# Performance work log

Hardware: AMD Instinct MI355X
Metric: run time of the kernel (lower is better)

Reference implementation:

```python
import jax, jax.numpy as jnp
import numpy as np
import math

EMBED_DIM = 1024
NUM_HEADS = 16
HEAD_DIM = EMBED_DIM // NUM_HEADS
B, S = 2, 2048


def setup_inputs() -> dict:
    key = jax.random.key(0)
    ks = jax.random.split(key, 5)
    scale = 1.0 / math.sqrt(EMBED_DIM)
    x = jax.random.normal(ks[0], (B, S, EMBED_DIM), dtype=jnp.float32)
    W_q = jax.random.normal(ks[1], (EMBED_DIM, EMBED_DIM), dtype=jnp.float32) * scale
    W_k = jax.random.normal(ks[2], (EMBED_DIM, EMBED_DIM), dtype=jnp.float32) * scale
    W_v = jax.random.normal(ks[3], (EMBED_DIM, EMBED_DIM), dtype=jnp.float32) * scale
    W_o = jax.random.normal(ks[4], (EMBED_DIM, EMBED_DIM), dtype=jnp.float32) * scale
    # causal mask: True = masked out (matches torch masked_fill semantics)
    mask = jnp.triu(jnp.ones((S, S), dtype=bool), k=1)
    return {"x": x, "mask": mask, "W_q": W_q, "W_k": W_k, "W_v": W_v, "W_o": W_o}


def _split_heads(x):
    b, s, _ = x.shape
    return x.reshape(b, s, NUM_HEADS, HEAD_DIM).transpose(0, 2, 1, 3)  # [b,h,s,hd]


def reference(x, mask, W_q, W_k, W_v, W_o):
    # torch nn.Linear(bias=False): y = x @ W.T
    Q = _split_heads(x @ W_q.T)
    K = _split_heads(x @ W_k.T)
    V = _split_heads(x @ W_v.T)
    scale = 1.0 / math.sqrt(HEAD_DIM)
    scores = jnp.einsum("bhqd,bhkd->bhqk", Q, K) * scale  # [b,h,s,s]
    scores = jnp.where(mask[None, None, :, :], -jnp.inf, scores)
    weights = jax.nn.softmax(scores, axis=-1)
    out = jnp.einsum("bhqk,bhkd->bhqd", weights, V)
    out = out.transpose(0, 2, 1, 3).reshape(x.shape[0], x.shape[1], EMBED_DIM)
    return out @ W_o.T
```

## Files before the change

### kernel.cpp

```cpp
#include <hip/hip_runtime.h>
#include <hip/hip_bf16.h>

typedef short bf16x8 __attribute__((ext_vector_type(8)));
typedef unsigned short u16x8 __attribute__((ext_vector_type(8)));
typedef float f32x4 __attribute__((ext_vector_type(4)));

typedef unsigned int __attribute__((address_space(1))) gu32;
typedef unsigned int __attribute__((address_space(3))) lu32;

#define MFMA16(a, b, c) __builtin_amdgcn_mfma_f32_16x16x32_bf16((a), (b), (c), 0, 0, 0)

constexpr int SEQ = 2048;
constexpr int NH = 16;
constexpr int NTOK = 2 * SEQ;

__device__ __forceinline__ float bf2f(unsigned short u) {
  union { unsigned int i; float f; } v; v.i = ((unsigned int)u) << 16; return v.f;
}
__device__ __forceinline__ unsigned short f2bf(float f) {
  __hip_bfloat16 h = __float2bfloat16(f);
  return __builtin_bit_cast(unsigned short, h);
}
__device__ __forceinline__ u16x8 cvt8(const float* __restrict__ p) {
  f32x4 a = *(const f32x4*)p;
  f32x4 b = *(const f32x4*)(p + 4);
  u16x8 r;
#pragma unroll
  for (int j = 0; j < 4; j++) { r[j] = f2bf(a[j]); r[4 + j] = f2bf(b[j]); }
  return r;
}

__global__ __launch_bounds__(256) void cvt_all(
    const float* __restrict__ x, const float* __restrict__ wq, const float* __restrict__ wk,
    const float* __restrict__ wv, const float* __restrict__ wo,
    unsigned short* __restrict__ Xb, unsigned short* __restrict__ Wb) {
  const int z = blockIdx.y;
  const float* src = (z == 0) ? x : (z == 1) ? wq : (z == 2) ? wk : (z == 3) ? wv : wo;
  unsigned short* dst = (z == 0) ? Xb : Wb + (size_t)(z - 1) * 1024 * 1024;
  const int n = (z == 0) ? NTOK * 1024 : 1024 * 1024;
  for (int i = (blockIdx.x * 256 + threadIdx.x) * 8; i < n; i += gridDim.x * 256 * 8)
    *(u16x8*)(dst + i) = cvt8(src + i);
}

template <int ROWS, int NWAVE>
__device__ __forceinline__ void stage_glds(const unsigned short* __restrict__ gbase,
                                           int rstride,
                                           unsigned short* __restrict__ lds,
                                           int wid, int lane) {
  constexpr int ISS = ROWS * 8 / (NWAVE * 64);
#pragma unroll
  for (int t = 0; t < ISS; ++t) {
    const int slot = (wid * ISS + t) * 64 + lane;
    const int row = slot >> 3;
    const int c8 = (slot & 7) ^ (row & 7);
    const unsigned short* gp = gbase + (size_t)row * rstride + c8 * 8;
    unsigned short* lp = lds + (size_t)(wid * ISS + t) * 512;
    __builtin_amdgcn_global_load_lds((const gu32*)gp, (lu32*)lp, 16, 0, 0);
  }
}

__device__ __forceinline__ bf16x8 frag_ld(const unsigned short* __restrict__ lds, int row, int c8) {
  const int slot = row * 8 + (c8 ^ (row & 7));
  return *(const bf16x8*)(lds + slot * 8);
}

template <int BM, int BN, int LDC, bool CF32>
__global__ __launch_bounds__(256) void gemm_lds(
    const unsigned short* __restrict__ A,
    const unsigned short* __restrict__ B,
    void* __restrict__ Cv) {
  constexpr int K = 1024;
  constexpr int MI = BM / 32, NI = BN / 32;

  __shared__ __align__(16) unsigned short As[BM * 64];
  __shared__ __align__(16) unsigned short Bs[BN * 64];

  const int tid = threadIdx.x;
  const int wid = tid >> 6;
  const int lane = tid & 63;
  const int quad = lane >> 4;
  const int c16 = lane & 15;
  const int wrow = wid >> 1, wcol = wid & 1;

  const int m0 = blockIdx.y * BM;
  const int n0 = blockIdx.x * BN;
  const unsigned short* Bz = B + (size_t)blockIdx.z * 1024 * 1024;
  const int cofs = blockIdx.z * 1024;

  f32x4 acc[MI][NI];
#pragma unroll
  for (int i = 0; i < MI; i++)
#pragma unroll
    for (int j = 0; j < NI; j++) acc[i][j] = f32x4{0.f, 0.f, 0.f, 0.f};

  for (int kb = 0; kb < K; kb += 64) {
    __syncthreads();
    stage_glds<BM, 4>(A + (size_t)m0 * K + kb, K, As, wid, lane);
    stage_glds<BN, 4>(Bz + (size_t)n0 * K + kb, K, Bs, wid, lane);
    __syncthreads();
#pragma unroll
    for (int ks = 0; ks < 2; ++ks) {
      bf16x8 af[MI], bfr[NI];
#pragma unroll
      for (int i = 0; i < MI; i++)
        af[i] = frag_ld(As, wrow * (BM / 2) + i * 16 + c16, ks * 4 + quad);
#pragma unroll
      for (int j = 0; j < NI; j++)
        bfr[j] = frag_ld(Bs, wcol * (BN / 2) + j * 16 + c16, ks * 4 + quad);
#pragma unroll
      for (int i = 0; i < MI; i++)
#pragma unroll
        for (int j = 0; j < NI; j++) acc[i][j] = MFMA16(af[i], bfr[j], acc[i][j]);
    }
  }

#pragma unroll
  for (int i = 0; i < MI; i++) {
#pragma unroll
    for (int j = 0; j < NI; j++) {
      int row = m0 + wrow * (BM / 2) + i * 16 + quad * 4;
      int col = n0 + wcol * (BN / 2) + j * 16 + c16 + cofs;
#pragma unroll
      for (int r = 0; r < 4; r++) {
        if constexpr (CF32) ((float*)Cv)[(size_t)(row + r) * LDC + col] = acc[i][j][r];
        else ((unsigned short*)Cv)[(size_t)(row + r) * LDC + col] = f2bf(acc[i][j][r]);
      }
    }
  }
}

__device__ __forceinline__ int vt_idx(int d, int kv) {
  int ck = kv >> 3;
  int s = ((d >> 3) ^ d) & 7;
  return d * 64 + ((ck ^ s) << 3) + (kv & 7);
}

struct AttnShared {
  unsigned short Kt[2][64 * 64];
  unsigned short Vt[2][64 * 64];
  unsigned short Pt[64][72];
};

__device__ __forceinline__ void attn_phase(
    AttnShared& sh, const unsigned short* __restrict__ QKV,
    unsigned short* __restrict__ Oa, size_t tokbase, int h, int q0, int nkv,
    int tid, int wid, int lane, int quad, int c16) {
  __syncthreads();

  const unsigned short* qp = QKV + (tokbase + q0 + wid * 16 + c16) * 3072 + h * 64;
  bf16x8 qf[2];
#pragma unroll
  for (int ks = 0; ks < 2; ++ks) {
    u16x8 u = *(const u16x8*)(qp + ks * 32 + quad * 8);
    bf16x8 t;
#pragma unroll
    for (int j = 0; j < 8; j++) t[j] = (short)f2bf(0.1803368801f * bf2f(u[j]));
    qf[ks] = t;
  }

  const unsigned short* kbase = QKV + tokbase * 3072 + 1024 + h * 64;
  const unsigned short* vbase = QKV + tokbase * 3072 + 2048 + h * 64;
  const int vrp = tid >> 3, vc8 = tid & 7;

  f32x4 o[4];
  float lacc[4];
#pragma unroll
  for (int nt = 0; nt < 4; nt++) o[nt] = f32x4{0.f, 0.f, 0.f, 0.f};
#pragma unroll
  for (int r = 0; r < 4; r++) lacc[r] = 0.f;

  stage_glds<64, 4>(kbase, 3072, sh.Kt[0], wid, lane);
  u16x8 vr0 = *(const u16x8*)(vbase + (size_t)(vrp * 2) * 3072 + vc8 * 8);
  u16x8 vr1 = *(const u16x8*)(vbase + (size_t)(vrp * 2 + 1) * 3072 + vc8 * 8);

  for (int kt = 0; kt < nkv; ++kt) {
    const int buf = kt & 1;
#pragma unroll
    for (int j = 0; j < 8; j++) {
      unsigned int w = (unsigned int)vr0[j] | ((unsigned int)vr1[j] << 16);
      *(unsigned int*)&sh.Vt[buf][vt_idx(vc8 * 8 + j, vrp * 2)] = w;
    }
    __syncthreads();

    if (kt + 1 < nkv) {
      const size_t nofs = (size_t)(kt + 1) * 64;
      stage_glds<64, 4>(kbase + nofs * 3072, 3072, sh.Kt[buf ^ 1], wid, lane);
      vr0 = *(const u16x8*)(vbase + (nofs + vrp * 2) * 3072 + vc8 * 8);
      vr1 = *(const u16x8*)(vbase + (nofs + vrp * 2 + 1) * 3072 + vc8 * 8);
    }

    const unsigned short* KtB = sh.Kt[buf];
    const unsigned short* VtB = sh.Vt[buf];
    f32x4 s[4];
#pragma unroll
    for (int nt = 0; nt < 4; ++nt) {
      f32x4 a = f32x4{-16.f, -16.f, -16.f, -16.f};
      a = MFMA16(qf[0], frag_ld(KtB, nt * 16 + c16, quad), a);
      a = MFMA16(qf[1], frag_ld(KtB, nt * 16 + c16, 4 + quad), a);
      s[nt] = a;
    }
    if (kt == nkv - 1) {
#pragma unroll
      for (int nt = 0; nt < 4; nt++)
#pragma unroll
        for (int r = 0; r < 4; r++) {
          int qg = wid * 16 + quad * 4 + r;
          int kg = nt * 16 + c16;
          if (kg > qg) s[nt][r] = -1e30f;
        }
    }

#pragma unroll
    for (int nt = 0; nt < 4; nt++) {
#pragma unroll
      for (int r = 0; r < 4; r++) {
        float p = exp2f(s[nt][r]);
        lacc[r] += p;
        sh.Pt[wid * 16 + quad * 4 + r][nt * 16 + c16] = f2bf(p);
      }
    }

#pragma unroll
    for (int ks = 0; ks < 2; ++ks) {
      bf16x8 pf = *(const bf16x8*)&sh.Pt[wid * 16 + c16][ks * 32 + quad * 8];
#pragma unroll
      for (int nt = 0; nt < 4; ++nt) {
        bf16x8 vf = *(const bf16x8*)&VtB[vt_idx(nt * 16 + c16, ks * 32 + quad * 8)];
        o[nt] = MFMA16(pf, vf, o[nt]);
      }
    }
  }

#pragma unroll
  for (int r = 0; r < 4; r++) {
#pragma unroll
    for (int off = 1; off < 16; off <<= 1) lacc[r] += __shfl_xor(lacc[r], off);
    lacc[r] = 1.f / lacc[r];
  }
#pragma unroll
  for (int nt = 0; nt < 4; nt++) {
#pragma unroll
    for (int r = 0; r < 4; r++) {
      int row = q0 + wid * 16 + quad * 4 + r;
      int col = h * 64 + nt * 16 + c16;
      Oa[(tokbase + row) * 1024 + col] = f2bf(o[nt][r] * lacc[r]);
    }
  }
}

__global__ __launch_bounds__(256) void attn_kernel(
    const unsigned short* __restrict__ QKV,
    unsigned short* __restrict__ Oa) {
  __shared__ AttnShared sh;
  const int pr = blockIdx.x;
  const int h = blockIdx.y;
  const int b = blockIdx.z;
  const int tid = threadIdx.x;
  const int wid = tid >> 6, lane = tid & 63;
  const int quad = lane >> 4, c16 = lane & 15;
  const size_t tokbase = (size_t)b * SEQ;

  attn_phase(sh, QKV, Oa, tokbase, h, (31 - pr) * 64, 32 - pr, tid, wid, lane, quad, c16);
  attn_phase(sh, QKV, Oa, tokbase, h, pr * 64, pr + 1, tid, wid, lane, quad, c16);
}

template <int BM, int BN, int LDC, bool AF32, bool CF32>
__global__ __launch_bounds__(256) void gemm_bt(
    const void* __restrict__ Av, const float* __restrict__ W0, const float* __restrict__ W1,
    const float* __restrict__ W2, void* __restrict__ Cv) {
  constexpr int K = 1024;
  constexpr int LDS_LD = 72;
  constexpr int MI = BM / 32, NI = BN / 32;
  __shared__ __align__(16) unsigned short As[BM][LDS_LD];
  __shared__ __align__(16) unsigned short Bs[BN][LDS_LD];
  const int tid = threadIdx.x, wid = tid >> 6, lane = tid & 63;
  const int quad = lane >> 4, c16 = lane & 15;
  const int wrow = wid >> 1, wcol = wid & 1;
  const float* W = (blockIdx.z == 0) ? W0 : (blockIdx.z == 1 ? W1 : W2);
  const int m0 = blockIdx.y * BM, n0 = blockIdx.x * BN, cofs = blockIdx.z * 1024;
  f32x4 acc[MI][NI];
#pragma unroll
  for (int i = 0; i < MI; i++)
#pragma unroll
    for (int j = 0; j < NI; j++) acc[i][j] = f32x4{0.f, 0.f, 0.f, 0.f};
  for (int kb = 0; kb < K; kb += 64) {
    __syncthreads();
#pragma unroll
    for (int c = tid; c < BM * 8; c += 256) {
      int row = c >> 3, c8 = c & 7;
      if constexpr (AF32)
        *(u16x8*)&As[row][c8 * 8] = cvt8((const float*)Av + (size_t)(m0 + row) * K + kb + c8 * 8);
      else
        *(u16x8*)&As[row][c8 * 8] = *(const u16x8*)((const unsigned short*)Av + (size_t)(m0 + row) * K + kb + c8 * 8);
    }
#pragma unroll
    for (int c = tid; c < BN * 8; c += 256) {
      int row = c >> 3, c8 = c & 7;
      *(u16x8*)&Bs[row][c8 * 8] = cvt8(W + (size_t)(n0 + row) * K + kb + c8 * 8);
    }
    __syncthreads();
#pragma unroll
    for (int ks = 0; ks < 2; ++ks) {
      bf16x8 af[MI], bfr[NI];
#pragma unroll
      for (int i = 0; i < MI; i++)
        af[i] = *(const bf16x8*)&As[wrow * (BM / 2) + i * 16 + c16][ks * 32 + quad * 8];
#pragma unroll
      for (int j = 0; j < NI; j++)
        bfr[j] = *(const bf16x8*)&Bs[wcol * (BN / 2) + j * 16 + c16][ks * 32 + quad * 8];
#pragma unroll
      for (int i = 0; i < MI; i++)
#pragma unroll
        for (int j = 0; j < NI; j++) acc[i][j] = MFMA16(af[i], bfr[j], acc[i][j]);
    }
  }
#pragma unroll
  for (int i = 0; i < MI; i++)
#pragma unroll
    for (int j = 0; j < NI; j++) {
      int row = m0 + wrow * (BM / 2) + i * 16 + quad * 4;
      int col = n0 + wcol * (BN / 2) + j * 16 + c16 + cofs;
#pragma unroll
      for (int r = 0; r < 4; r++) {
        if constexpr (CF32) ((float*)Cv)[(size_t)(row + r) * LDC + col] = acc[i][j][r];
        else ((unsigned short*)Cv)[(size_t)(row + r) * LDC + col] = f2bf(acc[i][j][r]);
      }
    }
}

extern "C" void kernel_launch(void* const* d_in, const int* in_sizes, int n_in,
                              void* d_out, int out_size, void* d_ws, size_t ws_size,
                              hipStream_t stream) {
  const float* x = (const float*)d_in[0];
  const float* Wq = (const float*)d_in[2];
  const float* Wk = (const float*)d_in[3];
  const float* Wv = (const float*)d_in[4];
  const float* Wo = (const float*)d_in[5];
  float* out = (float*)d_out;

  unsigned short* QKV = (unsigned short*)d_ws;
  unsigned short* Wb = QKV + (size_t)NTOK * 3072;
  unsigned short* Xb = Wb + (size_t)4 * 1024 * 1024;
  unsigned short* AT = Xb;

  if (ws_size >= (size_t)40 * 1024 * 1024) {
    cvt_all<<<dim3(256, 5), 256, 0, stream>>>(x, Wq, Wk, Wv, Wo, Xb, Wb);
    gemm_lds<128, 128, 3072, false><<<dim3(8, 32, 3), 256, 0, stream>>>(Xb, Wb, QKV);
    attn_kernel<<<dim3(16, NH, 2), 256, 0, stream>>>(QKV, AT);
    gemm_lds<128, 64, 1024, true><<<dim3(16, 32, 1), 256, 0, stream>>>(
        AT, Wb + (size_t)3 * 1024 * 1024, out);
  } else {
    unsigned short* QKV2 = (unsigned short*)d_ws;
    unsigned short* AT2 = QKV2 + (size_t)NTOK * 3072;
    gemm_bt<128, 128, 3072, true, false><<<dim3(8, 32, 3), 256, 0, stream>>>(x, Wq, Wk, Wv, QKV2);
    attn_kernel<<<dim3(16, NH, 2), 256, 0, stream>>>(QKV2, AT2);
    gemm_bt<64, 64, 1024, false, true><<<dim3(16, 64, 1), 256, 0, stream>>>(AT2, Wo, Wo, Wo, out);
  }
}
```

Measured before the change: 202.3 us.

## Use 2 waves per attention block, each computing 32 query rows

The attention kernel now runs 128 threads (2 waves) per block instead of 256 (4 waves), and each wave handles two 16-row query sub-tiles. Each K and V fragment loaded from LDS is therefore reused across two MFMA rows, which cuts LDS reads per FLOP. Staging of K/V is redistributed across the fewer threads. The cost is fewer waves per block for latency hiding, higher register pressure, and more per-thread staging work.

Measured after the change: 231.1 us. +14.3%, slower.

```diff
diff --git a/kernel.cpp b/kernel.cpp
--- a/kernel.cpp
+++ b/kernel.cpp
@@ -147,108 +147,139 @@
     int tid, int wid, int lane, int quad, int c16) {
   __syncthreads();
 
-  const unsigned short* qp = QKV + (tokbase + q0 + wid * 16 + c16) * 3072 + h * 64;
-  bf16x8 qf[2];
-#pragma unroll
-  for (int ks = 0; ks < 2; ++ks) {
-    u16x8 u = *(const u16x8*)(qp + ks * 32 + quad * 8);
-    bf16x8 t;
-#pragma unroll
-    for (int j = 0; j < 8; j++) t[j] = (short)f2bf(0.1803368801f * bf2f(u[j]));
-    qf[ks] = t;
+  const int qb = q0 + wid * 32;
+
+  bf16x8 qf[2][2];
+#pragma unroll
+  for (int m = 0; m < 2; ++m) {
+    const unsigned short* qp = QKV + (tokbase + qb + m * 16 + c16) * 3072 + h * 64;
+#pragma unroll
+    for (int ks = 0; ks < 2; ++ks) {
+      u16x8 u = *(const u16x8*)(qp + ks * 32 + quad * 8);
+      bf16x8 t;
+#pragma unroll
+      for (int j = 0; j < 8; j++) t[j] = (short)f2bf(0.1803368801f * bf2f(u[j]));
+      qf[m][ks] = t;
+    }
   }
 
   const unsigned short* kbase = QKV + tokbase * 3072 + 1024 + h * 64;
   const unsigned short* vbase = QKV + tokbase * 3072 + 2048 + h * 64;
-  const int vrp = tid >> 3, vc8 = tid & 7;
-
-  f32x4 o[4];
-  float lacc[4];
-#pragma unroll
-  for (int nt = 0; nt < 4; nt++) o[nt] = f32x4{0.f, 0.f, 0.f, 0.f};
-#pragma unroll
-  for (int r = 0; r < 4; r++) lacc[r] = 0.f;
-
-  stage_glds<64, 4>(kbase, 3072, sh.Kt[0], wid, lane);
-  u16x8 vr0 = *(const u16x8*)(vbase + (size_t)(vrp * 2) * 3072 + vc8 * 8);
-  u16x8 vr1 = *(const u16x8*)(vbase + (size_t)(vrp * 2 + 1) * 3072 + vc8 * 8);
+  const int vrg = tid >> 3, vc8 = tid & 7;
+
+  f32x4 o[2][4];
+  float lacc[2][4];
+#pragma unroll
+  for (int m = 0; m < 2; m++)
+#pragma unroll
+    for (int nt = 0; nt < 4; nt++) o[m][nt] = f32x4{0.f, 0.f, 0.f, 0.f};
+#pragma unroll
+  for (int m = 0; m < 2; m++)
+#pragma unroll
+    for (int r = 0; r < 4; r++) lacc[m][r] = 0.f;
+
+  stage_glds<64, 2>(kbase, 3072, sh.Kt[0], wid, lane);
+  u16x8 vr[4];
+#pragma unroll
+  for (int i = 0; i < 4; i++)
+    vr[i] = *(const u16x8*)(vbase + (size_t)(vrg * 4 + i) * 3072 + vc8 * 8);
 
   for (int kt = 0; kt < nkv; ++kt) {
     const int buf = kt & 1;
 #pragma unroll
-    for (int j = 0; j < 8; j++) {
-      unsigned int w = (unsigned int)vr0[j] | ((unsigned int)vr1[j] << 16);
-      *(unsigned int*)&sh.Vt[buf][vt_idx(vc8 * 8 + j, vrp * 2)] = w;
+    for (int i = 0; i < 4; i += 2) {
+#pragma unroll
+      for (int j = 0; j < 8; j++) {
+        unsigned int w = (unsigned int)vr[i][j] | ((unsigned int)vr[i + 1][j] << 16);
+        *(unsigned int*)&sh.Vt[buf][vt_idx(vc8 * 8 + j, vrg * 4 + i)] = w;
+      }
     }
     __syncthreads();
 
     if (kt + 1 < nkv) {
       const size_t nofs = (size_t)(kt + 1) * 64;
-      stage_glds<64, 4>(kbase + nofs * 3072, 3072, sh.Kt[buf ^ 1], wid, lane);
-      vr0 = *(const u16x8*)(vbase + (nofs + vrp * 2) * 3072 + vc8 * 8);
-      vr1 = *(const u16x8*)(vbase + (nofs + vrp * 2 + 1) * 3072 + vc8 * 8);
+      stage_glds<64, 2>(kbase + nofs * 3072, 3072, sh.Kt[buf ^ 1], wid, lane);
+#pragma unroll
+      for (int i = 0; i < 4; i++)
+        vr[i] = *(const u16x8*)(vbase + (nofs + vrg * 4 + i) * 3072 + vc8 * 8);
     }
 
     const unsigned short* KtB = sh.Kt[buf];
     const unsigned short* VtB = sh.Vt[buf];
-    f32x4 s[4];
+    f32x4 s[2][4];
 #pragma unroll
     for (int nt = 0; nt < 4; ++nt) {
-      f32x4 a = f32x4{-16.f, -16.f, -16.f, -16.f};
-      a = MFMA16(qf[0], frag_ld(KtB, nt * 16 + c16, quad), a);
-      a = MFMA16(qf[1], frag_ld(KtB, nt * 16 + c16, 4 + quad), a);
-      s[nt] = a;
+      bf16x8 k0 = frag_ld(KtB, nt * 16 + c16, quad);
+      bf16x8 k1 = frag_ld(KtB, nt * 16 + c16, 4 + quad);
+#pragma unroll
+      for (int m = 0; m < 2; ++m) {
+        f32x4 a = f32x4{-16.f, -16.f, -16.f, -16.f};
+        a = MFMA16(qf[m][0], k0, a);
+        a = MFMA16(qf[m][1], k1, a);
+        s[m][nt] = a;
+      }
     }
     if (kt == nkv - 1) {
+      const int kv0 = kt * 64;
+#pragma unroll
+      for (int m = 0; m < 2; m++)
+#pragma unroll
+        for (int nt = 0; nt < 4; nt++)
+#pragma unroll
+          for (int r = 0; r < 4; r++) {
+            int qg = qb + m * 16 + quad * 4 + r;
+            int kg = kv0 + nt * 16 + c16;
+            if (kg > qg) s[m][nt][r] = -1e30f;
+          }
+    }
+
+#pragma unroll
+    for (int m = 0; m < 2; m++)
 #pragma unroll
       for (int nt = 0; nt < 4; nt++)
 #pragma unroll
         for (int r = 0; r < 4; r++) {
-          int qg = wid * 16 + quad * 4 + r;
-          int kg = nt * 16 + c16;
-          if (kg > qg) s[nt][r] = -1e30f;
+          float p = exp2f(s[m][nt][r]);
+          lacc[m][r] += p;
+          sh.Pt[wid * 32 + m * 16 + quad * 4 + r][nt * 16 + c16] = f2bf(p);
         }
-    }
-
-#pragma unroll
-    for (int nt = 0; nt < 4; nt++) {
-#pragma unroll
-      for (int r = 0; r < 4; r++) {
-        float p = exp2f(s[nt][r]);
-        lacc[r] += p;
-        sh.Pt[wid * 16 + quad * 4 + r][nt * 16 + c16] = f2bf(p);
-      }
-    }
 
 #pragma unroll
     for (int ks = 0; ks < 2; ++ks) {
-      bf16x8 pf = *(const bf16x8*)&sh.Pt[wid * 16 + c16][ks * 32 + quad * 8];
+      bf16x8 pf[2];
+#pragma unroll
+      for (int m = 0; m < 2; m++)
+        pf[m] = *(const bf16x8*)&sh.Pt[wid * 32 + m * 16 + c16][ks * 32 + quad * 8];
 #pragma unroll
       for (int nt = 0; nt < 4; ++nt) {
         bf16x8 vf = *(const bf16x8*)&VtB[vt_idx(nt * 16 + c16, ks * 32 + quad * 8)];
-        o[nt] = MFMA16(pf, vf, o[nt]);
-      }
-    }
-  }
-
-#pragma unroll
-  for (int r = 0; r < 4; r++) {
-#pragma unroll
-    for (int off = 1; off < 16; off <<= 1) lacc[r] += __shfl_xor(lacc[r], off);
-    lacc[r] = 1.f / lacc[r];
-  }
-#pragma unroll
-  for (int nt = 0; nt < 4; nt++) {
+#pragma unroll
+        for (int m = 0; m < 2; m++) o[m][nt] = MFMA16(pf[m], vf, o[m][nt]);
+      }
+    }
+  }
+
+#pragma unroll
+  for (int m = 0; m < 2; m++)
 #pragma unroll
     for (int r = 0; r < 4; r++) {
-      int row = q0 + wid * 16 + quad * 4 + r;
-      int col = h * 64 + nt * 16 + c16;
-      Oa[(tokbase + row) * 1024 + col] = f2bf(o[nt][r] * lacc[r]);
-    }
-  }
-}
-
-__global__ __launch_bounds__(256) void attn_kernel(
+#pragma unroll
+      for (int off = 1; off < 16; off <<= 1) lacc[m][r] += __shfl_xor(lacc[m][r], off);
+      lacc[m][r] = 1.f / lacc[m][r];
+    }
+#pragma unroll
+  for (int m = 0; m < 2; m++)
+#pragma unroll
+    for (int nt = 0; nt < 4; nt++)
+#pragma unroll
+      for (int r = 0; r < 4; r++) {
+        int row = qb + m * 16 + quad * 4 + r;
+        int col = h * 64 + nt * 16 + c16;
+        Oa[(tokbase + row) * 1024 + col] = f2bf(o[m][nt][r] * lacc[m][r]);
+      }
+}
+
+__global__ __launch_bounds__(128) void attn_kernel(
     const unsigned short* __restrict__ QKV,
     unsigned short* __restrict__ Oa) {
   __shared__ AttnShared sh;
@@ -346,14 +377,14 @@
   if (ws_size >= (size_t)40 * 1024 * 1024) {
     cvt_all<<<dim3(256, 5), 256, 0, stream>>>(x, Wq, Wk, Wv, Wo, Xb, Wb);
     gemm_lds<128, 128, 3072, false><<<dim3(8, 32, 3), 256, 0, stream>>>(Xb, Wb, QKV);
-    attn_kernel<<<dim3(16, NH, 2), 256, 0, stream>>>(QKV, AT);
+    attn_kernel<<<dim3(16, NH, 2), 128, 0, stream>>>(QKV, AT);
     gemm_lds<128, 64, 1024, true><<<dim3(16, 32, 1), 256, 0, stream>>>(
         AT, Wb + (size_t)3 * 1024 * 1024, out);
   } else {
     unsigned short* QKV2 = (unsigned short*)d_ws;
     unsigned short* AT2 = QKV2 + (size_t)NTOK * 3072;
     gemm_bt<128, 128, 3072, true, false><<<dim3(8, 32, 3), 256, 0, stream>>>(x, Wq, Wk, Wv, QKV2);
-    attn_kernel<<<dim3(16, NH, 2), 256, 0, stream>>>(QKV2, AT2);
+    attn_kernel<<<dim3(16, NH, 2), 128, 0, stream>>>(QKV2, AT2);
     gemm_bt<64, 64, 1024, false, true><<<dim3(16, 64, 1), 256, 0, stream>>>(AT2, Wo, Wo, Wo, out);
   }
 }
```

## Shrink attention query tile to 32 rows with 128-thread blocks

Applied to the files above, without the earlier changes.

Halves the attention query tile from 64 to 32 rows per block and uses 2 waves (128 threads) instead of 4, doubling the grid to 32x16x2 blocks. V and K staging are re-split so each thread loads 4 V rows and K uses half the waves. The causal mask now uses global query and key indices because the 32-row tile no longer lines up with the 64-wide KV tile. This raises block count and occupancy, but each K/V tile loaded into LDS is now reused by fewer query rows.

Measured after the change: 216.5 us. +7.0%, slower.

```diff
diff --git a/kernel.cpp b/kernel.cpp
--- a/kernel.cpp
+++ b/kernel.cpp
@@ -138,7 +138,7 @@
 struct AttnShared {
   unsigned short Kt[2][64 * 64];
   unsigned short Vt[2][64 * 64];
-  unsigned short Pt[64][72];
+  unsigned short Pt[32][72];
 };
 
 __device__ __forceinline__ void attn_phase(
@@ -160,7 +160,7 @@
 
   const unsigned short* kbase = QKV + tokbase * 3072 + 1024 + h * 64;
   const unsigned short* vbase = QKV + tokbase * 3072 + 2048 + h * 64;
-  const int vrp = tid >> 3, vc8 = tid & 7;
+  const int vrg = tid >> 3, vc8 = tid & 7;
 
   f32x4 o[4];
   float lacc[4];
@@ -169,24 +169,30 @@
 #pragma unroll
   for (int r = 0; r < 4; r++) lacc[r] = 0.f;
 
-  stage_glds<64, 4>(kbase, 3072, sh.Kt[0], wid, lane);
-  u16x8 vr0 = *(const u16x8*)(vbase + (size_t)(vrp * 2) * 3072 + vc8 * 8);
-  u16x8 vr1 = *(const u16x8*)(vbase + (size_t)(vrp * 2 + 1) * 3072 + vc8 * 8);
+  stage_glds<64, 2>(kbase, 3072, sh.Kt[0], wid, lane);
+  u16x8 vr[4];
+#pragma unroll
+  for (int i = 0; i < 4; i++)
+    vr[i] = *(const u16x8*)(vbase + (size_t)(vrg * 4 + i) * 3072 + vc8 * 8);
 
   for (int kt = 0; kt < nkv; ++kt) {
     const int buf = kt & 1;
 #pragma unroll
-    for (int j = 0; j < 8; j++) {
-      unsigned int w = (unsigned int)vr0[j] | ((unsigned int)vr1[j] << 16);
-      *(unsigned int*)&sh.Vt[buf][vt_idx(vc8 * 8 + j, vrp * 2)] = w;
+    for (int i = 0; i < 4; i += 2) {
+#pragma unroll
+      for (int j = 0; j < 8; j++) {
+        unsigned int w = (unsigned int)vr[i][j] | ((unsigned int)vr[i + 1][j] << 16);
+        *(unsigned int*)&sh.Vt[buf][vt_idx(vc8 * 8 + j, vrg * 4 + i)] = w;
+      }
     }
     __syncthreads();
 
     if (kt + 1 < nkv) {
       const size_t nofs = (size_t)(kt + 1) * 64;
-      stage_glds<64, 4>(kbase + nofs * 3072, 3072, sh.Kt[buf ^ 1], wid, lane);
-      vr0 = *(const u16x8*)(vbase + (nofs + vrp * 2) * 3072 + vc8 * 8);
-      vr1 = *(const u16x8*)(vbase + (nofs + vrp * 2 + 1) * 3072 + vc8 * 8);
+      stage_glds<64, 2>(kbase + nofs * 3072, 3072, sh.Kt[buf ^ 1], wid, lane);
+#pragma unroll
+      for (int i = 0; i < 4; i++)
+        vr[i] = *(const u16x8*)(vbase + (nofs + vrg * 4 + i) * 3072 + vc8 * 8);
     }
 
     const unsigned short* KtB = sh.Kt[buf];
@@ -200,25 +206,25 @@
       s[nt] = a;
     }
     if (kt == nkv - 1) {
+      const int kv0 = kt * 64;
 #pragma unroll
       for (int nt = 0; nt < 4; nt++)
 #pragma unroll
         for (int r = 0; r < 4; r++) {
-          int qg = wid * 16 + quad * 4 + r;
-          int kg = nt * 16 + c16;
+          int qg = q0 + wid * 16 + quad * 4 + r;
+          int kg = kv0 + nt * 16 + c16;
           if (kg > qg) s[nt][r] = -1e30f;
         }
     }
 
 #pragma unroll
-    for (int nt = 0; nt < 4; nt++) {
+    for (int nt = 0; nt < 4; nt++)
 #pragma unroll
       for (int r = 0; r < 4; r++) {
         float p = exp2f(s[nt][r]);
         lacc[r] += p;
         sh.Pt[wid * 16 + quad * 4 + r][nt * 16 + c16] = f2bf(p);
       }
-    }
 
 #pragma unroll
     for (int ks = 0; ks < 2; ++ks) {
@@ -238,17 +244,16 @@
     lacc[r] = 1.f / lacc[r];
   }
 #pragma unroll
-  for (int nt = 0; nt < 4; nt++) {
+  for (int nt = 0; nt < 4; nt++)
 #pragma unroll
     for (int r = 0; r < 4; r++) {
       int row = q0 + wid * 16 + quad * 4 + r;
       int col = h * 64 + nt * 16 + c16;
       Oa[(tokbase + row) * 1024 + col] = f2bf(o[nt][r] * lacc[r]);
     }
-  }
-}
-
-__global__ __launch_bounds__(256) void attn_kernel(
+}
+
+__global__ __launch_bounds__(128) void attn_kernel(
     const unsigned short* __restrict__ QKV,
     unsigned short* __restrict__ Oa) {
   __shared__ AttnShared sh;
@@ -260,8 +265,10 @@
   const int quad = lane >> 4, c16 = lane & 15;
   const size_t tokbase = (size_t)b * SEQ;
 
-  attn_phase(sh, QKV, Oa, tokbase, h, (31 - pr) * 64, 32 - pr, tid, wid, lane, quad, c16);
-  attn_phase(sh, QKV, Oa, tokbase, h, pr * 64, pr + 1, tid, wid, lane, quad, c16);
+  const int tA = 63 - pr;
+  const int tB = pr;
+  attn_phase(sh, QKV, Oa, tokbase, h, tA * 32, tA / 2 + 1, tid, wid, lane, quad, c16);
+  attn_phase(sh, QKV, Oa, tokbase, h, tB * 32, tB / 2 + 1, tid, wid, lane, quad, c16);
 }
 
 template <int BM, int BN, int LDC, bool AF32, bool CF32>
@@ -346,14 +353,14 @@
   if (ws_size >= (size_t)40 * 1024 * 1024) {
     cvt_all<<<dim3(256, 5), 256, 0, stream>>>(x, Wq, Wk, Wv, Wo, Xb, Wb);
     gemm_lds<128, 128, 3072, false><<<dim3(8, 32, 3), 256, 0, stream>>>(Xb, Wb, QKV);
-    attn_kernel<<<dim3(16, NH, 2), 256, 0, stream>>>(QKV, AT);
+    attn_kernel<<<dim3(32, NH, 2), 128, 0, stream>>>(QKV, AT);
     gemm_lds<128, 64, 1024, true><<<dim3(16, 32, 1), 256, 0, stream>>>(
         AT, Wb + (size_t)3 * 1024 * 1024, out);
   } else {
     unsigned short* QKV2 = (unsigned short*)d_ws;
     unsigned short* AT2 = QKV2 + (size_t)NTOK * 3072;
     gemm_bt<128, 128, 3072, true, false><<<dim3(8, 32, 3), 256, 0, stream>>>(x, Wq, Wk, Wv, QKV2);
-    attn_kernel<<<dim3(16, NH, 2), 256, 0, stream>>>(QKV2, AT2);
+    attn_kernel<<<dim3(32, NH, 2), 128, 0, stream>>>(QKV2, AT2);
     gemm_bt<64, 64, 1024, false, true><<<dim3(16, 64, 1), 256, 0, stream>>>(AT2, Wo, Wo, Wo, out);
   }
 }
```

## Transpose attention MFMA operands so rows stay per-lane and writes vectorize

Applied to the files above, without the earlier changes.

Swaps the A/B operands of both attention MFMAs so each lane holds a query row along c16 and four consecutive kv or d values in its accumulator. This lets P be written to a per-wave LDS tile with 8-byte stores, makes the row sum a per-lane scalar reduced with two shuffles instead of four 4-step reductions, and makes output stores packed 8-byte writes. The V transpose staging is also rewritten to 4x4 blocks with uint2 LDS stores. The causal mask indexing changes to match the new layout, so any mistake there would break correctness.

After: 205.8 us. About the same (+1.7%).

```diff
diff --git a/kernel.cpp b/kernel.cpp
--- a/kernel.cpp
+++ b/kernel.cpp
@@ -3,6 +3,7 @@
 
 typedef short bf16x8 __attribute__((ext_vector_type(8)));
 typedef unsigned short u16x8 __attribute__((ext_vector_type(8)));
+typedef unsigned short u16x4 __attribute__((ext_vector_type(4)));
 typedef float f32x4 __attribute__((ext_vector_type(4)));
 
 typedef unsigned int __attribute__((address_space(1))) gu32;
@@ -138,7 +139,7 @@
 struct AttnShared {
   unsigned short Kt[2][64 * 64];
   unsigned short Vt[2][64 * 64];
-  unsigned short Pt[64][72];
+  unsigned short Pt[4][16 * 72];
 };
 
 __device__ __forceinline__ void attn_phase(
@@ -160,91 +161,96 @@
 
   const unsigned short* kbase = QKV + tokbase * 3072 + 1024 + h * 64;
   const unsigned short* vbase = QKV + tokbase * 3072 + 2048 + h * 64;
-  const int vrp = tid >> 3, vc8 = tid & 7;
+  const int vkv = (tid >> 4) * 4;
+  const int vd = (tid & 15) * 4;
 
   f32x4 o[4];
-  float lacc[4];
+  float lacc = 0.f;
 #pragma unroll
   for (int nt = 0; nt < 4; nt++) o[nt] = f32x4{0.f, 0.f, 0.f, 0.f};
-#pragma unroll
-  for (int r = 0; r < 4; r++) lacc[r] = 0.f;
+  unsigned short* PtW = sh.Pt[wid];
 
   stage_glds<64, 4>(kbase, 3072, sh.Kt[0], wid, lane);
-  u16x8 vr0 = *(const u16x8*)(vbase + (size_t)(vrp * 2) * 3072 + vc8 * 8);
-  u16x8 vr1 = *(const u16x8*)(vbase + (size_t)(vrp * 2 + 1) * 3072 + vc8 * 8);
+  u16x4 vr[4];
+#pragma unroll
+  for (int i = 0; i < 4; i++)
+    vr[i] = *(const u16x4*)(vbase + (size_t)(vkv + i) * 3072 + vd);
 
   for (int kt = 0; kt < nkv; ++kt) {
     const int buf = kt & 1;
 #pragma unroll
-    for (int j = 0; j < 8; j++) {
-      unsigned int w = (unsigned int)vr0[j] | ((unsigned int)vr1[j] << 16);
-      *(unsigned int*)&sh.Vt[buf][vt_idx(vc8 * 8 + j, vrp * 2)] = w;
+    for (int dd = 0; dd < 4; ++dd) {
+      uint2 w;
+      w.x = (unsigned int)vr[0][dd] | ((unsigned int)vr[1][dd] << 16);
+      w.y = (unsigned int)vr[2][dd] | ((unsigned int)vr[3][dd] << 16);
+      *(uint2*)&sh.Vt[buf][vt_idx(vd + dd, vkv)] = w;
     }
     __syncthreads();
 
     if (kt + 1 < nkv) {
       const size_t nofs = (size_t)(kt + 1) * 64;
       stage_glds<64, 4>(kbase + nofs * 3072, 3072, sh.Kt[buf ^ 1], wid, lane);
-      vr0 = *(const u16x8*)(vbase + (nofs + vrp * 2) * 3072 + vc8 * 8);
-      vr1 = *(const u16x8*)(vbase + (nofs + vrp * 2 + 1) * 3072 + vc8 * 8);
+#pragma unroll
+      for (int i = 0; i < 4; i++)
+        vr[i] = *(const u16x4*)(vbase + (nofs + vkv + i) * 3072 + vd);
     }
 
     const unsigned short* KtB = sh.Kt[buf];
     const unsigned short* VtB = sh.Vt[buf];
-    f32x4 s[4];
+    f32x4 st[4];
 #pragma unroll
     for (int nt = 0; nt < 4; ++nt) {
       f32x4 a = f32x4{-16.f, -16.f, -16.f, -16.f};
-      a = MFMA16(qf[0], frag_ld(KtB, nt * 16 + c16, quad), a);
-      a = MFMA16(qf[1], frag_ld(KtB, nt * 16 + c16, 4 + quad), a);
-      s[nt] = a;
+      a = MFMA16(frag_ld(KtB, nt * 16 + c16, quad), qf[0], a);
+      a = MFMA16(frag_ld(KtB, nt * 16 + c16, 4 + quad), qf[1], a);
+      st[nt] = a;
     }
     if (kt == nkv - 1) {
+      const int kv0 = kt * 64;
+      const int qg = q0 + wid * 16 + c16;
 #pragma unroll
       for (int nt = 0; nt < 4; nt++)
 #pragma unroll
         for (int r = 0; r < 4; r++) {
-          int qg = wid * 16 + quad * 4 + r;
-          int kg = nt * 16 + c16;
-          if (kg > qg) s[nt][r] = -1e30f;
+          int kg = kv0 + nt * 16 + quad * 4 + r;
+          if (kg > qg) st[nt][r] = -1e30f;
         }
     }
 
 #pragma unroll
     for (int nt = 0; nt < 4; nt++) {
-#pragma unroll
-      for (int r = 0; r < 4; r++) {
-        float p = exp2f(s[nt][r]);
-        lacc[r] += p;
-        sh.Pt[wid * 16 + quad * 4 + r][nt * 16 + c16] = f2bf(p);
+      float p0 = exp2f(st[nt][0]);
+      float p1 = exp2f(st[nt][1]);
+      float p2 = exp2f(st[nt][2]);
+      float p3 = exp2f(st[nt][3]);
+      lacc += (p0 + p1) + (p2 + p3);
+      uint2 w;
+      w.x = (unsigned int)f2bf(p0) | ((unsigned int)f2bf(p1) << 16);
+      w.y = (unsigned int)f2bf(p2) | ((unsigned int)f2bf(p3) << 16);
+      *(uint2*)&PtW[c16 * 72 + nt * 16 + quad * 4] = w;
+    }
+
+#pragma unroll
+    for (int ks = 0; ks < 2; ++ks) {
+      bf16x8 pf = *(const bf16x8*)&PtW[c16 * 72 + ks * 32 + quad * 8];
+#pragma unroll
+      for (int nt2 = 0; nt2 < 4; ++nt2) {
+        bf16x8 vf = *(const bf16x8*)&VtB[vt_idx(nt2 * 16 + c16, ks * 32 + quad * 8)];
+        o[nt2] = MFMA16(vf, pf, o[nt2]);
       }
     }
-
-#pragma unroll
-    for (int ks = 0; ks < 2; ++ks) {
-      bf16x8 pf = *(const bf16x8*)&sh.Pt[wid * 16 + c16][ks * 32 + quad * 8];
-#pragma unroll
-      for (int nt = 0; nt < 4; ++nt) {
-        bf16x8 vf = *(const bf16x8*)&VtB[vt_idx(nt * 16 + c16, ks * 32 + quad * 8)];
-        o[nt] = MFMA16(pf, vf, o[nt]);
-      }
-    }
-  }
-
-#pragma unroll
-  for (int r = 0; r < 4; r++) {
-#pragma unroll
-    for (int off = 1; off < 16; off <<= 1) lacc[r] += __shfl_xor(lacc[r], off);
-    lacc[r] = 1.f / lacc[r];
-  }
-#pragma unroll
-  for (int nt = 0; nt < 4; nt++) {
-#pragma unroll
-    for (int r = 0; r < 4; r++) {
-      int row = q0 + wid * 16 + quad * 4 + r;
-      int col = h * 64 + nt * 16 + c16;
-      Oa[(tokbase + row) * 1024 + col] = f2bf(o[nt][r] * lacc[r]);
-    }
+  }
+
+  lacc += __shfl_xor(lacc, 16);
+  lacc += __shfl_xor(lacc, 32);
+  const float linv = 1.f / lacc;
+  const size_t row = tokbase + q0 + wid * 16 + c16;
+#pragma unroll
+  for (int nt2 = 0; nt2 < 4; nt2++) {
+    uint2 w;
+    w.x = (unsigned int)f2bf(o[nt2][0] * linv) | ((unsigned int)f2bf(o[nt2][1] * linv) << 16);
+    w.y = (unsigned int)f2bf(o[nt2][2] * linv) | ((unsigned int)f2bf(o[nt2][3] * linv) << 16);
+    *(uint2*)&Oa[row * 1024 + h * 64 + nt2 * 16 + quad * 4] = w;
   }
 }
 
@@ -260,8 +266,10 @@
   const int quad = lane >> 4, c16 = lane & 15;
   const size_t tokbase = (size_t)b * SEQ;
 
-  attn_phase(sh, QKV, Oa, tokbase, h, (31 - pr) * 64, 32 - pr, tid, wid, lane, quad, c16);
-  attn_phase(sh, QKV, Oa, tokbase, h, pr * 64, pr + 1, tid, wid, lane, quad, c16);
+  const int tA = 31 - pr;
+  const int tB = pr;
+  attn_phase(sh, QKV, Oa, tokbase, h, tA * 64, tA + 1, tid, wid, lane, quad, c16);
+  attn_phase(sh, QKV, Oa, tokbase, h, tB * 64, tB + 1, tid, wid, lane, quad, c16);
 }
 
 template <int BM, int BN, int LDC, bool AF32, bool CF32>
```
